# Kernel tuning notes

Measured on AMD Instinct MI355X. Metric: run time of the kernel, lower is better.

Reference implementation:

```python
import jax, jax.numpy as jnp
import numpy as np

D = 2048      # token_dim (forced equal to visual feat dim by concat shapes)
V = 10000     # vocab size
B = 32        # batch
X = 36        # regions
T = 20        # max_len / caption length
FEAT = 2048


def setup_inputs() -> dict:
    key = jax.random.key(0)
    ks = jax.random.split(key, 20)
    s = 0.02
    inp = {
        "features": jax.random.normal(ks[0], (B, X, FEAT), jnp.float32),
        "caption": jax.random.randint(ks[1], (B, T), 0, V),
        "emb": jax.random.normal(ks[2], (V, D), jnp.float32) * s,
        # attention LSTMCell: input 3*D, hidden D
        "Wih_a": jax.random.normal(ks[3], (4 * D, 3 * D), jnp.float32) * s,
        "Whh_a": jax.random.normal(ks[4], (4 * D, D), jnp.float32) * s,
        "bih_a": jnp.zeros((4 * D,), jnp.float32),
        "bhh_a": jnp.zeros((4 * D,), jnp.float32),
        # language LSTMCell: input 2*D, hidden D
        "Wih_l": jax.random.normal(ks[5], (4 * D, 2 * D), jnp.float32) * s,
        "Whh_l": jax.random.normal(ks[6], (4 * D, D), jnp.float32) * s,
        "bih_l": jnp.zeros((4 * D,), jnp.float32),
        "bhh_l": jnp.zeros((4 * D,), jnp.float32),
        # attention MLP
        "Wv": jax.random.normal(ks[7], (D, FEAT), jnp.float32) * s,
        "bv": jnp.zeros((D,), jnp.float32),
        "Wh": jax.random.normal(ks[8], (D, D), jnp.float32) * s,
        "bh": jnp.zeros((D,), jnp.float32),
        "Wa": jax.random.normal(ks[9], (1, D), jnp.float32) * s,
        "ba": jnp.zeros((1,), jnp.float32),
        # output projection
        "Wfc": jax.random.normal(ks[10], (V, D), jnp.float32) * s,
        "bfc": jnp.zeros((V,), jnp.float32),
    }
    return inp


def _lstm_cell(x, h, c, Wih, Whh, bih, bhh):
    # PyTorch LSTMCell: gates in (i, f, g, o) order
    z = x @ Wih.T + bih + h @ Whh.T + bhh
    i, f, g, o = jnp.split(z, 4, axis=-1)
    c_new = jax.nn.sigmoid(f) * c + jax.nn.sigmoid(i) * jnp.tanh(g)
    h_new = jax.nn.sigmoid(o) * jnp.tanh(c_new)
    return h_new, c_new


def reference(features, caption, emb, Wih_a, Whh_a, bih_a, bhh_a,
              Wih_l, Whh_l, bih_l, bhh_l, Wv, bv, Wh, bh, Wa, ba, Wfc, bfc):
    v_bar = jnp.mean(features, axis=1)            # [B, 2048]
    embs = emb[caption]                            # [B, T, D]
    a_v = features @ Wv.T + bv                     # [B, X, D], t-invariant

    h0 = jnp.zeros((features.shape[0], D), features.dtype)
    carry0 = (h0, h0, h0, h0)  # (h_attn, c_attn, h_lang, c_lang)

    def step(carry, e_t):
        h_a, c_a, h_l, c_l = carry
        x = jnp.concatenate([h_l, v_bar, e_t], axis=1)          # [B, 3D]
        h_a, c_a = _lstm_cell(x, h_a, c_a, Wih_a, Whh_a, bih_a, bhh_a)
        # additive attention (NB: softmax over trailing singleton dim,
        # reproduced faithfully from the source -> weights are all ones)
        a_h = (h_a @ Wh.T + bh)[:, None, :]                      # [B, 1, D]
        a = jnp.tanh(a_v + a_h) @ Wa.T + ba                      # [B, X, 1]
        a_w = jax.nn.softmax(a, axis=-1)                         # [B, X, 1]
        v_hat = jnp.sum(a_w * features, axis=1)                  # [B, 2048]
        x2 = jnp.concatenate([h_a, v_hat], axis=1)               # [B, 2D]
        h_l, c_l = _lstm_cell(x2, h_l, c_l, Wih_l, Whh_l, bih_l, bhh_l)
        logits_t = h_l @ Wfc.T + bfc                             # [B, V]
        return (h_a, c_a, h_l, c_l), logits_t

    _, logits = jax.lax.scan(step, carry0, jnp.swapaxes(embs, 0, 1))  # [T, B, V]
    logits = jnp.swapaxes(logits, 0, 1)                               # [B, T, V]
    return jax.nn.log_softmax(logits, axis=2)
```

## Files before the change

kernel.cpp:

```cpp
#include <hip/hip_runtime.h>

typedef unsigned short u16;
typedef __attribute__((ext_vector_type(8))) short bf16x8;
typedef __attribute__((ext_vector_type(4))) float f32x4;

#define DD 2048
#define VV 10000
#define BB 32
#define TT 20

__device__ __forceinline__ u16 f2bf(float f) {
    unsigned u = __float_as_uint(f);
    u += 0x7fffu + ((u >> 16) & 1u);
    return (u16)(u >> 16);
}
__device__ __forceinline__ float bf2f(u16 h) {
    return __uint_as_float(((unsigned)h) << 16);
}

__global__ __launch_bounds__(256) void cast_weights(
    const float* __restrict__ Wih_a, const float* __restrict__ Whh_a,
    const float* __restrict__ Wih_l, const float* __restrict__ Whh_l,
    const float* __restrict__ Wfc,
    u16* __restrict__ Wcat_a, u16* __restrict__ Wcat_l, u16* __restrict__ Wfc_b)
{
    const long long S1 = 8192LL * 4096;
    const long long S3 = 20480000LL;
    long long g = (long long)blockIdx.x * 256 + threadIdx.x;
    long long e = g * 4;
    const float* src;
    u16* dst;
    if (e < S1) {
        int n = (int)(e >> 12), k = (int)(e & 4095);
        src = (k < 2048) ? (Wih_a + (size_t)n * 6144 + k)
                         : (Whh_a + (size_t)n * 2048 + (k - 2048));
        dst = Wcat_a + e;
    } else if (e < 2 * S1) {
        long long e2 = e - S1;
        int n = (int)(e2 >> 12), k = (int)(e2 & 4095);
        src = (k < 2048) ? (Wih_l + (size_t)n * 4096 + k)
                         : (Whh_l + (size_t)n * 2048 + (k - 2048));
        dst = Wcat_l + e2;
    } else {
        long long e3 = e - 2 * S1;
        if (e3 >= S3) return;
        src = Wfc + e3;
        dst = Wfc_b + e3;
    }
    float4 v = *(const float4*)src;
    ushort4 o;
    o.x = f2bf(v.x); o.y = f2bf(v.y); o.z = f2bf(v.z); o.w = f2bf(v.w);
    *(ushort4*)dst = o;
}

__global__ __launch_bounds__(256) void prep(
    const float* __restrict__ features,
    u16* __restrict__ vbar, u16* __restrict__ vhat,
    float* __restrict__ c_a, float* __restrict__ c_l,
    u16* __restrict__ Ha0, u16* __restrict__ Hl0)
{
    int i = blockIdx.x * 256 + threadIdx.x;
    int b = i >> 11, d = i & 2047;
    const float* f = features + (size_t)b * 36 * 2048 + d;
    float s = 0.f;
#pragma unroll
    for (int x = 0; x < 36; ++x) s += f[(size_t)x * 2048];
    vhat[i] = f2bf(s);
    vbar[i] = f2bf(s * (1.f / 36.f));
    c_a[i] = 0.f; c_l[i] = 0.f;
    Ha0[i] = 0;  Hl0[i] = 0;
}

__global__ __launch_bounds__(256) void embed_k(
    const float* __restrict__ emb, const int* __restrict__ caption,
    u16* __restrict__ embs)
{
    int i = blockIdx.x * 256 + threadIdx.x;
    int m = i >> 11, d = i & 2047;
    int t = m >> 5, b = m & 31;
    int tok = caption[b * TT + t];
    embs[i] = f2bf(emb[(size_t)tok * 2048 + d]);
}

template <int MT>
__global__ __launch_bounds__(256) void pre_gemm(
    const u16* __restrict__ A, const float* __restrict__ W,
    int ldw, int kofs,
    const float* __restrict__ bias0, const float* __restrict__ bias1,
    const float* __restrict__ addend, float* __restrict__ out)
{
    const int lane = threadIdx.x & 63;
    const int wv = threadIdx.x >> 6;
    const int lr = lane & 15, lq = lane >> 4;
    const int n0 = blockIdx.x * 64 + wv * 16;
    const int m0 = blockIdx.y * (MT * 16);

    f32x4 acc[MT];
#pragma unroll
    for (int i = 0; i < MT; ++i) acc[i] = (f32x4){0.f, 0.f, 0.f, 0.f};

    const float* wrow = W + (size_t)(n0 + lr) * ldw + kofs + lq * 8;
    const u16* arow = A + (size_t)(m0 + lr) * 2048 + lq * 8;

    for (int k = 0; k < 2048; k += 32) {
        float4 wlo = *(const float4*)(wrow + k);
        float4 whi = *(const float4*)(wrow + k + 4);
        bf16x8 bf;
        bf[0] = (short)f2bf(wlo.x); bf[1] = (short)f2bf(wlo.y);
        bf[2] = (short)f2bf(wlo.z); bf[3] = (short)f2bf(wlo.w);
        bf[4] = (short)f2bf(whi.x); bf[5] = (short)f2bf(whi.y);
        bf[6] = (short)f2bf(whi.z); bf[7] = (short)f2bf(whi.w);
#pragma unroll
        for (int mt = 0; mt < MT; ++mt) {
            bf16x8 af = *(const bf16x8*)(arow + (size_t)mt * 16 * 2048 + k);
            acc[mt] = __builtin_amdgcn_mfma_f32_16x16x32_bf16(af, bf, acc[mt], 0, 0, 0);
        }
    }
    const int n = n0 + lr;
    float badd = 0.f;
    if (bias0) badd += bias0[n];
    if (bias1) badd += bias1[n];
#pragma unroll
    for (int mt = 0; mt < MT; ++mt) {
#pragma unroll
        for (int r = 0; r < 4; ++r) {
            int m = m0 + mt * 16 + lq * 4 + r;
            float v = acc[mt][r] + badd;
            if (addend) v += addend[(size_t)(m & 31) * 8192 + n];
            out[(size_t)m * 8192 + n] = v;
        }
    }
}

__global__ __launch_bounds__(512) void step_kernel(
    const u16* __restrict__ A0, const u16* __restrict__ A1,
    const u16* __restrict__ W, const float* __restrict__ zconst,
    float* __restrict__ c, u16* __restrict__ hout)
{
    __shared__ float zred[4][32][64];
    const int lane = threadIdx.x & 63;
    const int w = threadIdx.x >> 6;
    const int lr = lane & 15, lq = lane >> 4;
    const int d0 = blockIdx.x * 16;

    const u16* Aptr = (w < 4) ? A0 : A1;
    const int kA = (w & 3) * 512 + lq * 8;
    const int kW = w * 512 + lq * 8;

    f32x4 acc[2][4];
#pragma unroll
    for (int m = 0; m < 2; ++m)
#pragma unroll
        for (int g = 0; g < 4; ++g) acc[m][g] = (f32x4){0.f, 0.f, 0.f, 0.f};

    const u16* a_row0 = Aptr + (size_t)lr * 2048 + kA;
    const u16* a_row1 = Aptr + (size_t)(16 + lr) * 2048 + kA;
    const u16* b_row[4];
#pragma unroll
    for (int g = 0; g < 4; ++g)
        b_row[g] = W + (size_t)(g * 2048 + d0 + lr) * 4096 + kW;

    for (int kk = 0; kk < 512; kk += 32) {
        bf16x8 a0 = *(const bf16x8*)(a_row0 + kk);
        bf16x8 a1 = *(const bf16x8*)(a_row1 + kk);
#pragma unroll
        for (int g = 0; g < 4; ++g) {
            bf16x8 bf = *(const bf16x8*)(b_row[g] + kk);
            acc[0][g] = __builtin_amdgcn_mfma_f32_16x16x32_bf16(a0, bf, acc[0][g], 0, 0, 0);
            acc[1][g] = __builtin_amdgcn_mfma_f32_16x16x32_bf16(a1, bf, acc[1][g], 0, 0, 0);
        }
    }

    if (w >= 4) {
#pragma unroll
        for (int m = 0; m < 2; ++m)
#pragma unroll
            for (int g = 0; g < 4; ++g)
#pragma unroll
                for (int r = 0; r < 4; ++r)
                    zred[w - 4][m * 16 + lq * 4 + r][g * 16 + lr] = acc[m][g][r];
    }
    __syncthreads();
    if (w < 4) {
#pragma unroll
        for (int m = 0; m < 2; ++m)
#pragma unroll
            for (int g = 0; g < 4; ++g)
#pragma unroll
                for (int r = 0; r < 4; ++r)
                    zred[w][m * 16 + lq * 4 + r][g * 16 + lr] += acc[m][g][r];
    }
    __syncthreads();

    const int b = threadIdx.x >> 4;
    const int j = threadIdx.x & 15;
    const int d = d0 + j;
    float z[4];
#pragma unroll
    for (int g = 0; g < 4; ++g) {
        float s = zconst[(size_t)b * 8192 + g * 2048 + d];
#pragma unroll
        for (int wv = 0; wv < 4; ++wv) s += zred[wv][b][g * 16 + j];
        z[g] = s;
    }
    float ig = 1.f / (1.f + __expf(-z[0]));
    float fg = 1.f / (1.f + __expf(-z[1]));
    float gg = tanhf(z[2]);
    float og = 1.f / (1.f + __expf(-z[3]));
    float cn = fg * c[(size_t)b * 2048 + d] + ig * gg;
    c[(size_t)b * 2048 + d] = cn;
    hout[(size_t)b * 2048 + d] = f2bf(og * tanhf(cn));
}

template <int MT>
__global__ __launch_bounds__(256) void logits_gemm(
    const u16* __restrict__ A, const u16* __restrict__ Wb,
    const float* __restrict__ bias, float* __restrict__ out)
{
    const int lane = threadIdx.x & 63;
    const int wv = threadIdx.x >> 6;
    const int lr = lane & 15, lq = lane >> 4;
    const int n0 = blockIdx.x * 64 + wv * 16;
    if (n0 >= VV) return;
    const int m0 = blockIdx.y * (MT * 16);

    f32x4 acc[MT];
#pragma unroll
    for (int i = 0; i < MT; ++i) acc[i] = (f32x4){0.f, 0.f, 0.f, 0.f};

    const u16* wrow = Wb + (size_t)(n0 + lr) * 2048 + lq * 8;
    const u16* arow = A + (size_t)(m0 + lr) * 2048 + lq * 8;

    for (int k = 0; k < 2048; k += 32) {
        bf16x8 bf = *(const bf16x8*)(wrow + k);
#pragma unroll
        for (int mt = 0; mt < MT; ++mt) {
            bf16x8 af = *(const bf16x8*)(arow + (size_t)mt * 16 * 2048 + k);
            acc[mt] = __builtin_amdgcn_mfma_f32_16x16x32_bf16(af, bf, acc[mt], 0, 0, 0);
        }
    }
    const int n = n0 + lr;
    const float bv = bias[n];
#pragma unroll
    for (int mt = 0; mt < MT; ++mt) {
#pragma unroll
        for (int r = 0; r < 4; ++r) {
            int m = m0 + mt * 16 + lq * 4 + r;
            int t = m >> 5, b = m & 31;
            out[(size_t)b * (TT * VV) + (size_t)t * VV + n] = acc[mt][r] + bv;
        }
    }
}

__global__ __launch_bounds__(256) void logsoftmax(float* __restrict__ out)
{
    float* p = out + (size_t)blockIdx.x * VV;
    const int tid = threadIdx.x, lane = tid & 63, wv = tid >> 6;
    __shared__ float red[4], red2[4];
    float mx = -1e30f;
    for (int i = tid; i < VV; i += 256) mx = fmaxf(mx, p[i]);
    for (int o = 32; o > 0; o >>= 1) mx = fmaxf(mx, __shfl_down(mx, o, 64));
    if (lane == 0) red[wv] = mx;
    __syncthreads();
    mx = fmaxf(fmaxf(red[0], red[1]), fmaxf(red[2], red[3]));
    float sum = 0.f;
    for (int i = tid; i < VV; i += 256) sum += __expf(p[i] - mx);
    for (int o = 32; o > 0; o >>= 1) sum += __shfl_down(sum, o, 64);
    if (lane == 0) red2[wv] = sum;
    __syncthreads();
    sum = red2[0] + red2[1] + red2[2] + red2[3];
    const float lse = mx + __logf(sum);
    for (int i = tid; i < VV; i += 256) p[i] = p[i] - lse;
}

extern "C" void kernel_launch(void* const* d_in, const int* in_sizes, int n_in,
                              void* d_out, int out_size, void* d_ws, size_t ws_size,
                              hipStream_t stream)
{
    const float* features = (const float*)d_in[0];
    const int*   caption  = (const int*)d_in[1];
    const float* emb      = (const float*)d_in[2];
    const float* Wih_a    = (const float*)d_in[3];
    const float* Whh_a    = (const float*)d_in[4];
    const float* bih_a    = (const float*)d_in[5];
    const float* bhh_a    = (const float*)d_in[6];
    const float* Wih_l    = (const float*)d_in[7];
    const float* Whh_l    = (const float*)d_in[8];
    const float* bih_l    = (const float*)d_in[9];
    const float* bhh_l    = (const float*)d_in[10];
    const float* Wfc      = (const float*)d_in[17];
    const float* bfc      = (const float*)d_in[18];
    float* out = (float*)d_out;

    char* ws = (char*)d_ws;
    size_t off = 0;
    auto alloc = [&](size_t bytes) { void* p = ws + off; off += (bytes + 255) & ~(size_t)255; return p; };
    u16* Wcat_a  = (u16*)alloc(8192ull * 4096 * 2);
    u16* Wcat_l  = (u16*)alloc(8192ull * 4096 * 2);
    u16* Wfc_b   = (u16*)alloc(10000ull * 2048 * 2);
    float* z_const = (float*)alloc(20ull * 32 * 8192 * 4);
    float* const_a = (float*)alloc(32ull * 8192 * 4);
    float* const_l = (float*)alloc(32ull * 8192 * 4);
    u16* embs    = (u16*)alloc(640ull * 2048 * 2);
    u16* vbar    = (u16*)alloc(32ull * 2048 * 2);
    u16* vhat    = (u16*)alloc(32ull * 2048 * 2);
    u16* Ha      = (u16*)alloc(2ull * 32 * 2048 * 2);
    u16* Hl      = (u16*)alloc(21ull * 32 * 2048 * 2);
    float* c_a   = (float*)alloc(32ull * 2048 * 4);
    float* c_l   = (float*)alloc(32ull * 2048 * 4);
    (void)ws_size; (void)in_sizes; (void)n_in; (void)out_size;

    cast_weights<<<dim3(85536), dim3(256), 0, stream>>>(
        Wih_a, Whh_a, Wih_l, Whh_l, Wfc, Wcat_a, Wcat_l, Wfc_b);
    prep<<<dim3(256), dim3(256), 0, stream>>>(features, vbar, vhat, c_a, c_l, Ha, Hl);
    embed_k<<<dim3(5120), dim3(256), 0, stream>>>(emb, caption, embs);
    pre_gemm<2><<<dim3(128, 1), dim3(256), 0, stream>>>(
        vbar, Wih_a, 6144, 2048, bih_a, bhh_a, nullptr, const_a);
    pre_gemm<2><<<dim3(128, 1), dim3(256), 0, stream>>>(
        vhat, Wih_l, 4096, 2048, bih_l, bhh_l, nullptr, const_l);
    pre_gemm<10><<<dim3(128, 4), dim3(256), 0, stream>>>(
        embs, Wih_a, 6144, 4096, nullptr, nullptr, const_a, z_const);

    for (int t = 0; t < 20; ++t) {
        u16* hl_prev = Hl + (size_t)t * 65536;
        u16* ha_prev = Ha + (size_t)(t & 1) * 65536;
        u16* ha_new  = Ha + (size_t)((t + 1) & 1) * 65536;
        u16* hl_new  = Hl + (size_t)(t + 1) * 65536;
        step_kernel<<<dim3(128), dim3(512), 0, stream>>>(
            hl_prev, ha_prev, Wcat_a, z_const + (size_t)t * 262144, c_a, ha_new);
        step_kernel<<<dim3(128), dim3(512), 0, stream>>>(
            ha_new, hl_prev, Wcat_l, const_l, c_l, hl_new);
    }

    logits_gemm<10><<<dim3(157, 4), dim3(256), 0, stream>>>(Hl + 65536, Wfc_b, bfc, out);
    logsoftmax<<<dim3(640), dim3(256), 0, stream>>>(out);
}
```

Before: 2.049 ms.

## Split recurrent step GEMM across 512 blocks with 4 hidden units each

The per-step LSTM kernel now uses 512 blocks of 256 threads, each covering 4 hidden units across all 4 gates, packed into one 16-row MFMA tile. Each wave handles a 1024-wide K slice instead of 512, with a smaller shared-memory reduction. The goal is to spread the weight streaming of the latency-bound recurrent steps over more CUs. Separately, the precompute and logits GEMMs use 20 M-tiles per block with half as many grid rows, trading parallelism for more weight reuse.

```diff
diff --git a/kernel.cpp b/kernel.cpp
--- a/kernel.cpp
+++ b/kernel.cpp
@@ -13,9 +13,6 @@
     unsigned u = __float_as_uint(f);
     u += 0x7fffu + ((u >> 16) & 1u);
     return (u16)(u >> 16);
-}
-__device__ __forceinline__ float bf2f(u16 h) {
-    return __uint_as_float(((unsigned)h) << 16);
 }
 
 __global__ __launch_bounds__(256) void cast_weights(
@@ -132,84 +129,65 @@
     }
 }
 
-__global__ __launch_bounds__(512) void step_kernel(
+__global__ __launch_bounds__(256) void step_kernel(
     const u16* __restrict__ A0, const u16* __restrict__ A1,
     const u16* __restrict__ W, const float* __restrict__ zconst,
     float* __restrict__ c, u16* __restrict__ hout)
 {
-    __shared__ float zred[4][32][64];
+    __shared__ float zred[4][32][17];
     const int lane = threadIdx.x & 63;
     const int w = threadIdx.x >> 6;
     const int lr = lane & 15, lq = lane >> 4;
-    const int d0 = blockIdx.x * 16;
-
-    const u16* Aptr = (w < 4) ? A0 : A1;
-    const int kA = (w & 3) * 512 + lq * 8;
-    const int kW = w * 512 + lq * 8;
-
-    f32x4 acc[2][4];
-#pragma unroll
-    for (int m = 0; m < 2; ++m)
-#pragma unroll
-        for (int g = 0; g < 4; ++g) acc[m][g] = (f32x4){0.f, 0.f, 0.f, 0.f};
+    const int d0 = blockIdx.x * 4;
+
+    const u16* Aptr = (w < 2) ? A0 : A1;
+    const int kA = (w & 1) * 1024 + lq * 8;
+    const int kW = w * 1024 + lq * 8;
+
+    f32x4 acc0 = (f32x4){0.f, 0.f, 0.f, 0.f};
+    f32x4 acc1 = (f32x4){0.f, 0.f, 0.f, 0.f};
 
     const u16* a_row0 = Aptr + (size_t)lr * 2048 + kA;
     const u16* a_row1 = Aptr + (size_t)(16 + lr) * 2048 + kA;
-    const u16* b_row[4];
-#pragma unroll
-    for (int g = 0; g < 4; ++g)
-        b_row[g] = W + (size_t)(g * 2048 + d0 + lr) * 4096 + kW;
-
-    for (int kk = 0; kk < 512; kk += 32) {
+    const int wrow = (lr >> 2) * 2048 + d0 + (lr & 3);
+    const u16* b_ptr = W + (size_t)wrow * 4096 + kW;
+
+#pragma unroll 4
+    for (int kk = 0; kk < 1024; kk += 32) {
+        bf16x8 bf = *(const bf16x8*)(b_ptr + kk);
         bf16x8 a0 = *(const bf16x8*)(a_row0 + kk);
         bf16x8 a1 = *(const bf16x8*)(a_row1 + kk);
+        acc0 = __builtin_amdgcn_mfma_f32_16x16x32_bf16(a0, bf, acc0, 0, 0, 0);
+        acc1 = __builtin_amdgcn_mfma_f32_16x16x32_bf16(a1, bf, acc1, 0, 0, 0);
+    }
+
+#pragma unroll
+    for (int r = 0; r < 4; ++r) {
+        zred[w][lq * 4 + r][lr] = acc0[r];
+        zred[w][16 + lq * 4 + r][lr] = acc1[r];
+    }
+    __syncthreads();
+
+    if (threadIdx.x < 128) {
+        const int b = threadIdx.x >> 2;
+        const int j = threadIdx.x & 3;
+        const int d = d0 + j;
+        float z[4];
 #pragma unroll
         for (int g = 0; g < 4; ++g) {
-            bf16x8 bf = *(const bf16x8*)(b_row[g] + kk);
-            acc[0][g] = __builtin_amdgcn_mfma_f32_16x16x32_bf16(a0, bf, acc[0][g], 0, 0, 0);
-            acc[1][g] = __builtin_amdgcn_mfma_f32_16x16x32_bf16(a1, bf, acc[1][g], 0, 0, 0);
-        }
-    }
-
-    if (w >= 4) {
-#pragma unroll
-        for (int m = 0; m < 2; ++m)
-#pragma unroll
-            for (int g = 0; g < 4; ++g)
-#pragma unroll
-                for (int r = 0; r < 4; ++r)
-                    zred[w - 4][m * 16 + lq * 4 + r][g * 16 + lr] = acc[m][g][r];
-    }
-    __syncthreads();
-    if (w < 4) {
-#pragma unroll
-        for (int m = 0; m < 2; ++m)
-#pragma unroll
-            for (int g = 0; g < 4; ++g)
-#pragma unroll
-                for (int r = 0; r < 4; ++r)
-                    zred[w][m * 16 + lq * 4 + r][g * 16 + lr] += acc[m][g][r];
-    }
-    __syncthreads();
-
-    const int b = threadIdx.x >> 4;
-    const int j = threadIdx.x & 15;
-    const int d = d0 + j;
-    float z[4];
-#pragma unroll
-    for (int g = 0; g < 4; ++g) {
-        float s = zconst[(size_t)b * 8192 + g * 2048 + d];
-#pragma unroll
-        for (int wv = 0; wv < 4; ++wv) s += zred[wv][b][g * 16 + j];
-        z[g] = s;
-    }
-    float ig = 1.f / (1.f + __expf(-z[0]));
-    float fg = 1.f / (1.f + __expf(-z[1]));
-    float gg = tanhf(z[2]);
-    float og = 1.f / (1.f + __expf(-z[3]));
-    float cn = fg * c[(size_t)b * 2048 + d] + ig * gg;
-    c[(size_t)b * 2048 + d] = cn;
-    hout[(size_t)b * 2048 + d] = f2bf(og * tanhf(cn));
+            float s = zconst[(size_t)b * 8192 + g * 2048 + d];
+#pragma unroll
+            for (int wv = 0; wv < 4; ++wv) s += zred[wv][b][g * 4 + j];
+            z[g] = s;
+        }
+        float ig = 1.f / (1.f + __expf(-z[0]));
+        float fg = 1.f / (1.f + __expf(-z[1]));
+        float gg = tanhf(z[2]);
+        float og = 1.f / (1.f + __expf(-z[3]));
+        float cn = fg * c[(size_t)b * 2048 + d] + ig * gg;
+        c[(size_t)b * 2048 + d] = cn;
+        hout[(size_t)b * 2048 + d] = f2bf(og * tanhf(cn));
+    }
 }
 
 template <int MT>
@@ -318,7 +296,7 @@
         vbar, Wih_a, 6144, 2048, bih_a, bhh_a, nullptr, const_a);
     pre_gemm<2><<<dim3(128, 1), dim3(256), 0, stream>>>(
         vhat, Wih_l, 4096, 2048, bih_l, bhh_l, nullptr, const_l);
-    pre_gemm<10><<<dim3(128, 4), dim3(256), 0, stream>>>(
+    pre_gemm<20><<<dim3(128, 2), dim3(256), 0, stream>>>(
         embs, Wih_a, 6144, 4096, nullptr, nullptr, const_a, z_const);
 
     for (int t = 0; t < 20; ++t) {
@@ -326,12 +304,12 @@
         u16* ha_prev = Ha + (size_t)(t & 1) * 65536;
         u16* ha_new  = Ha + (size_t)((t + 1) & 1) * 65536;
         u16* hl_new  = Hl + (size_t)(t + 1) * 65536;
-        step_kernel<<<dim3(128), dim3(512), 0, stream>>>(
+        step_kernel<<<dim3(512), dim3(256), 0, stream>>>(
             hl_prev, ha_prev, Wcat_a, z_const + (size_t)t * 262144, c_a, ha_new);
-        step_kernel<<<dim3(128), dim3(512), 0, stream>>>(
+        step_kernel<<<dim3(512), dim3(256), 0, stream>>>(
             ha_new, hl_prev, Wcat_l, const_l, c_l, hl_new);
     }
 
-    logits_gemm<10><<<dim3(157, 4), dim3(256), 0, stream>>>(Hl + 65536, Wfc_b, bfc, out);
+    logits_gemm<20><<<dim3(157, 2), dim3(256), 0, stream>>>(Hl + 65536, Wfc_b, bfc, out);
     logsoftmax<<<dim3(640), dim3(256), 0, stream>>>(out);
 }
```

Measured after the change: 2.146 ms. 1.05x slower.
